# Kernel tuning notes

Measured on AMD Instinct MI355X. Metric: run time of the kernel, lower is better.

The kernel has to match this reference:

```python
import jax, jax.numpy as jnp
import numpy as np

NV = [12544, 6272, 3136, 1568, 784]  # vertex counts, fine -> coarse
SPIRAL = 9


def _grid_sample(im, grid):
    """Faithful port of the hand-rolled bilinear_grid_sample, align_corners=True.
    im: (n, c, h, w); grid: (n, gh, gw, 2) in [-1, 1]. Returns (n, c, gh*gw)."""
    n, c, h, w = im.shape
    gx = grid[..., 0].reshape(n, -1)
    gy = grid[..., 1].reshape(n, -1)
    x = (gx + 1) / 2 * (w - 1)
    y = (gy + 1) / 2 * (h - 1)
    x0 = jnp.floor(x); y0 = jnp.floor(y)
    x1 = x0 + 1; y1 = y0 + 1
    wa = (x1 - x) * (y1 - y)
    wb = (x1 - x) * (y - y0)
    wc = (x - x0) * (y1 - y)
    wd = (x - x0) * (y - y0)
    imp = jnp.pad(im, ((0, 0), (0, 0), (1, 1), (1, 1)))  # explicit zero pad as in source
    ph, pw = h + 2, w + 2
    x0i = jnp.clip(x0.astype(jnp.int32) + 1, 0, pw - 1)
    x1i = jnp.clip(x1.astype(jnp.int32) + 1, 0, pw - 1)
    y0i = jnp.clip(y0.astype(jnp.int32) + 1, 0, ph - 1)
    y1i = jnp.clip(y1.astype(jnp.int32) + 1, 0, ph - 1)
    impf = imp.reshape(n, c, -1)

    def gat(xi, yi):
        idx = xi + yi * pw  # (n, P)
        return jnp.take_along_axis(impf, idx[:, None, :], axis=2)  # (n, c, P)

    Ia = gat(x0i, y0i); Ib = gat(x0i, y1i); Ic = gat(x1i, y0i); Id = gat(x1i, y1i)
    return Ia * wa[:, None] + Ib * wb[:, None] + Ic * wc[:, None] + Id * wd[:, None]


def _pool(x, col, val):
    """Mesh up-pooling: gather columns, weight, and 3-way sum per output vertex.
    With row = repeat(arange(n_out), 3) the row_map built in __init__ is exactly
    arange(3*n_out).reshape(n_out, 3), so the three gathers reduce to reshape+sum."""
    out = x[:, col, :] * val[None, :, None]  # (B, 3*n_out, C)
    n_out = val.shape[0] // 3
    return out.reshape(x.shape[0], n_out, 3, x.shape[2]).sum(axis=2)


def _dsconv(x, idx, dw, pw):
    """Depthwise-separable spiral conv: gather spiral neighborhood, depthwise
    conv over spiral dim (per-channel), then 1x1 pointwise projection."""
    gsp = x[:, idx, :]                        # (B, N, S, Cin)
    y = jnp.einsum('bnsc,cs->bnc', gsp, dw)   # depthwise over spiral
    return y @ pw                             # (B, N, Cout)


def setup_inputs() -> dict:
    key = jax.random.key(0)
    ks = jax.random.split(key, 32)
    d = {}
    d['uv'] = jax.random.uniform(ks[0], (16, 64, 2), jnp.float32)
    d['feat'] = jax.random.normal(ks[1], (16, 256, 4, 4), jnp.float32)
    d['upsample'] = jax.random.normal(ks[2], (NV[4], 64), jnp.float32) * 0.01
    chs = [(256, 256), (256, 256), (256, 128), (128, 64)]
    for i, (ci, co) in enumerate(chs):
        d['dw%d' % i] = jax.random.normal(ks[3 + 2 * i], (ci, SPIRAL), jnp.float32) * (1.0 / SPIRAL)
        d['pw%d' % i] = jax.random.normal(ks[4 + 2 * i], (ci, co), jnp.float32) * (ci ** -0.5)
    d['dw_head'] = jax.random.normal(ks[11], (64, SPIRAL), jnp.float32) * (1.0 / SPIRAL)
    d['pw_head'] = jax.random.normal(ks[12], (64, 3), jnp.float32) * (64 ** -0.5)
    for j in range(4):
        n_out, n_in = NV[j], NV[j + 1]
        d['sp_idx_%d' % j] = jax.random.randint(ks[13 + j], (NV[j], SPIRAL), 0, NV[j], dtype=jnp.int32)
        d['up_col_%d' % j] = jax.random.randint(ks[17 + j], (3 * n_out,), 0, n_in, dtype=jnp.int32)
        d['up_val_%d' % j] = jax.random.uniform(ks[21 + j], (3 * n_out,), jnp.float32)
    return d


def reference(uv, feat, upsample, dw0, pw0, dw1, pw1, dw2, pw2, dw3, pw3, dw_head, pw_head,
              up_val_0, up_val_1, up_val_2, up_val_3,
              sp_idx_0, sp_idx_1, sp_idx_2, sp_idx_3,
              up_col_0, up_col_1, up_col_2, up_col_3):
    g = jnp.clip((uv - 0.5) * 2.0, -1.0, 1.0)[:, :, None, :]  # (B, P, 1, 2)
    x = _grid_sample(feat, g)            # (B, 256, P)
    x = x.transpose(0, 2, 1)             # (B, P, 256)
    x = jnp.einsum('vp,bpc->bvc', upsample, x)  # (B, 784, 256) coarse mesh feats
    specs = [(up_col_3, up_val_3, sp_idx_3, dw0, pw0),
             (up_col_2, up_val_2, sp_idx_2, dw1, pw1),
             (up_col_1, up_val_1, sp_idx_1, dw2, pw2),
             (up_col_0, up_val_0, sp_idx_0, dw3, pw3)]
    for col, val, idx, dw, pw in specs:
        x = _pool(x, col, val)
        x = jax.nn.relu(_dsconv(x, idx, dw, pw))
    return _dsconv(x, sp_idx_0, dw_head, pw_head)  # (B, 12544, 3)
```

## Files before the change

kernel.cpp:

```cpp
#include <hip/hip_runtime.h>


typedef _Float16 half8 __attribute__((ext_vector_type(8)));
typedef float    f32x4 __attribute__((ext_vector_type(4)));

__device__ __forceinline__ float4 ld4(const float* p) { return *(const float4*)p; }

__device__ __forceinline__ float lo16f(unsigned u) {
  _Float16 h; unsigned short s = (unsigned short)(u & 0xffffu);
  __builtin_memcpy(&h, &s, 2); return (float)h;
}
__device__ __forceinline__ float hi16f(unsigned u) {
  _Float16 h; unsigned short s = (unsigned short)(u >> 16);
  __builtin_memcpy(&h, &s, 2); return (float)h;
}
__device__ __forceinline__ float h2f(unsigned short s) {
  _Float16 h; __builtin_memcpy(&h, &s, 2); return (float)h;
}
__device__ __forceinline__ unsigned short hbits(float v) {
  _Float16 h = (_Float16)v; unsigned short u; __builtin_memcpy(&u, &h, 2); return u;
}
__device__ __forceinline__ unsigned pk2h(float a, float b) {
  return (unsigned)hbits(a) | ((unsigned)hbits(b) << 16);
}
__device__ __forceinline__ void split2h(float v, unsigned short& h, unsigned short& l) {
  _Float16 hf = (_Float16)v;
  float hif = (float)hf;
  _Float16 lf = (_Float16)((v - hif) * 2048.0f);
  __builtin_memcpy(&h, &hf, 2); __builtin_memcpy(&l, &lf, 2);
}
__device__ __forceinline__ void gload_lds16(const unsigned short* g, unsigned short* l) {
  __builtin_amdgcn_global_load_lds(
      (const __attribute__((address_space(1))) unsigned int*)g,
      (__attribute__((address_space(3))) unsigned int*)l, 16, 0, 0);
}

__global__ __launch_bounds__(256) void k_prep(
    const float* __restrict__ pw0, const float* __restrict__ pw1,
    const float* __restrict__ pw2, const float* __restrict__ pw3,
    unsigned short* __restrict__ dst)
{
  const int b = blockIdx.x, t = threadIdx.x;
  const float* src; int ci_sh, co, f, off;
  if (b < 256)      { src = pw0; ci_sh = 8; co = 256; f = b*256 + t;       off = 0; }
  else if (b < 512) { src = pw1; ci_sh = 8; co = 256; f = (b-256)*256 + t; off = 65536; }
  else if (b < 640) { src = pw2; ci_sh = 8; co = 128; f = (b-512)*256 + t; off = 131072; }
  else              { src = pw3; ci_sh = 7; co = 64;  f = (b-640)*256 + t; off = 163840; }
  const int n = f >> ci_sh, k = f & ((1 << ci_sh) - 1);
  float v = src[(size_t)k*co + n];
  unsigned short h, l; split2h(v, h, l);
  dst[off + f]          = h;
  dst[172032 + off + f] = l;
}

__global__ __launch_bounds__(256) void k_prep_head(
    const float* __restrict__ dwh, const float* __restrict__ pwh,
    unsigned short* __restrict__ dst)
{
  const int i = blockIdx.x*256 + threadIdx.x;
  const int n = i >> 6, c = i & 63;
  float v = 0.f;
  if (n < 27) v = dwh[c*9 + n/3] * pwh[c*3 + n%3];
  unsigned short h, l; split2h(v, h, l);
  dst[i] = h; dst[2048 + i] = l;
}

__global__ __launch_bounds__(256) void k_prep_dw(
    const float* __restrict__ dw0, const float* __restrict__ dw1,
    const float* __restrict__ dw2, const float* __restrict__ dw3,
    float* __restrict__ dst)
{
  const int i = blockIdx.x*256 + threadIdx.x;
  if (i >= 8064) return;
  const float* src; int rel, C, off;
  if (i < 2304)      { src = dw0; rel = i;        C = 256; off = 0; }
  else if (i < 4608) { src = dw1; rel = i - 2304; C = 256; off = 2304; }
  else if (i < 6912) { src = dw2; rel = i - 4608; C = 256; off = 4608; }
  else               { src = dw3; rel = i - 6912; C = 128; off = 6912; }
  const int s = rel / C, c = rel % C;
  dst[off + rel] = src[c*9 + s];
}

__global__ __launch_bounds__(256) void k_samp(
    const float* __restrict__ uv, const float* __restrict__ feat,
    unsigned short* __restrict__ xs)
{
  __shared__ float feat_l[256][17];
  const int tid = threadIdx.x;
  const int b   = blockIdx.x;

  const float* fr = feat + ((size_t)b*256 + tid)*16;
  #pragma unroll
  for (int i = 0; i < 16; i += 4) {
    float4 f = ld4(fr + i);
    feat_l[tid][i+0] = f.x; feat_l[tid][i+1] = f.y;
    feat_l[tid][i+2] = f.z; feat_l[tid][i+3] = f.w;
  }
  #pragma unroll 4
  for (int p = 0; p < 64; ++p) {
    float gx = uv[((size_t)b*64 + p)*2 + 0];
    float gy = uv[((size_t)b*64 + p)*2 + 1];
    gx = fminf(fmaxf((gx - 0.5f)*2.f, -1.f), 1.f);
    gy = fminf(fmaxf((gy - 0.5f)*2.f, -1.f), 1.f);
    float x = (gx + 1.f)*0.5f*3.f;
    float y = (gy + 1.f)*0.5f*3.f;
    float fx = floorf(x), fy = floorf(y);
    int ix0 = (int)fx, iy0 = (int)fy;
    float wx = x - fx, wy = y - fy;
    int ix1 = ix0 + 1 > 3 ? 3 : ix0 + 1;
    int iy1 = iy0 + 1 > 3 ? 3 : iy0 + 1;
    float v00 = feat_l[tid][iy0*4+ix0];
    float v01 = feat_l[tid][iy0*4+ix1];
    float v10 = feat_l[tid][iy1*4+ix0];
    float v11 = feat_l[tid][iy1*4+ix1];
    float xv = (1.f-wy)*((1.f-wx)*v00 + wx*v01) + wy*((1.f-wx)*v10 + wx*v11);
    xs[((size_t)b*64 + p)*256 + tid] = hbits(xv);
  }
}

__global__ __launch_bounds__(256) void k_up(
    const unsigned short* __restrict__ xs, const float* __restrict__ up,
    unsigned short* __restrict__ x0)
{
  const int tid = threadIdx.x;
  const int b   = blockIdx.y;
  const int v0  = blockIdx.x * 16;

  float acc[16];
  #pragma unroll
  for (int i = 0; i < 16; ++i) acc[i] = 0.f;

  #pragma unroll 8
  for (int p = 0; p < 64; ++p) {
    const float xv = h2f(xs[((size_t)b*64 + p)*256 + tid]);
    #pragma unroll
    for (int i = 0; i < 16; ++i)
      acc[i] += up[(size_t)(v0+i)*64 + p] * xv;
  }
  #pragma unroll
  for (int i = 0; i < 16; ++i)
    x0[((size_t)b*784 + v0 + i)*256 + tid] = hbits(acc[i]);
}

template<int C>
__global__ __launch_bounds__(256) void k_pool(
    const unsigned short* __restrict__ x, const int* __restrict__ col,
    const float* __restrict__ val, unsigned short* __restrict__ out,
    int Vin, int Vout)
{
  constexpr int KGc = C/8;
  constexpr int UPB = 2*KGc;
  const int bp = blockIdx.x & 7;
  const int v0 = (blockIdx.x >> 3) * 8;
  const int t  = threadIdx.x;

  #pragma unroll
  for (int i = 0; i < (8*UPB)/256; ++i) {
    const int id = t + i*256;
    const int vl = id / UPB;
    const int rem = id - vl*UPB;
    const int bl = rem / KGc;
    const int kg = rem - bl*KGc;
    const int v  = v0 + vl;
    const int b  = 2*bp + bl;
    const int c0 = col[3*v+0], c1 = col[3*v+1], c2 = col[3*v+2];
    const float w0 = val[3*v+0], w1 = val[3*v+1], w2 = val[3*v+2];
    const uint4 A = *(const uint4*)(x + ((size_t)b*Vin + c0)*C + 8*kg);
    const uint4 B = *(const uint4*)(x + ((size_t)b*Vin + c1)*C + 8*kg);
    const uint4 Cv= *(const uint4*)(x + ((size_t)b*Vin + c2)*C + 8*kg);
    uint4 R;
    R.x = pk2h(w0*lo16f(A.x)+w1*lo16f(B.x)+w2*lo16f(Cv.x),
               w0*hi16f(A.x)+w1*hi16f(B.x)+w2*hi16f(Cv.x));
    R.y = pk2h(w0*lo16f(A.y)+w1*lo16f(B.y)+w2*lo16f(Cv.y),
               w0*hi16f(A.y)+w1*hi16f(B.y)+w2*hi16f(Cv.y));
    R.z = pk2h(w0*lo16f(A.z)+w1*lo16f(B.z)+w2*lo16f(Cv.z),
               w0*hi16f(A.z)+w1*hi16f(B.z)+w2*hi16f(Cv.z));
    R.w = pk2h(w0*lo16f(A.w)+w1*lo16f(B.w)+w2*lo16f(Cv.w),
               w0*hi16f(A.w)+w1*hi16f(B.w)+w2*hi16f(Cv.w));
    *(uint4*)(out + ((size_t)b*Vout + v)*C + 8*kg) = R;
  }
}

template<int CI>
__global__ __launch_bounds__(256) void k_dw(
    const unsigned short* __restrict__ pin, const int* __restrict__ idx,
    const float* __restrict__ dwT, unsigned short* __restrict__ aout, int V)
{
  constexpr int KG  = CI/8;
  constexpr int VPB = (CI==256) ? 8 : 16;
  constexpr int HV  = VPB/2;

  const int t    = threadIdx.x;
  const int bp   = blockIdx.x & 7;
  const int vg   = blockIdx.x >> 3;
  const int kg   = t & (KG - 1);
  const int rest = t / KG;
  const int bl   = rest & 1;
  const int vbase= rest >> 1;
  const int va   = vg*VPB + vbase;
  const int vb2  = va + HV;
  const int b    = 2*bp + bl;

  const unsigned short* base = pin + (size_t)b*V*CI + 8*kg;
  float y0[8], y1[8];
  #pragma unroll
  for (int j = 0; j < 8; ++j) { y0[j] = 0.f; y1[j] = 0.f; }

  #pragma unroll
  for (int s = 0; s < 9; ++s) {
    const float4 wa = *(const float4*)(dwT + s*CI + 8*kg);
    const float4 wb = *(const float4*)(dwT + s*CI + 8*kg + 4);
    const uint4 g0 = *(const uint4*)(base + (size_t)idx[va *9 + s]*CI);
    const uint4 g1 = *(const uint4*)(base + (size_t)idx[vb2*9 + s]*CI);
    y0[0] += wa.x*lo16f(g0.x); y0[1] += wa.y*hi16f(g0.x);
    y0[2] += wa.z*lo16f(g0.y); y0[3] += wa.w*hi16f(g0.y);
    y0[4] += wb.x*lo16f(g0.z); y0[5] += wb.y*hi16f(g0.z);
    y0[6] += wb.z*lo16f(g0.w); y0[7] += wb.w*hi16f(g0.w);
    y1[0] += wa.x*lo16f(g1.x); y1[1] += wa.y*hi16f(g1.x);
    y1[2] += wa.z*lo16f(g1.y); y1[3] += wa.w*hi16f(g1.y);
    y1[4] += wb.x*lo16f(g1.z); y1[5] += wb.y*hi16f(g1.z);
    y1[6] += wb.z*lo16f(g1.w); y1[7] += wb.w*hi16f(g1.w);
  }
  uint4 p0, p1;
  p0.x = pk2h(y0[0], y0[1]); p0.y = pk2h(y0[2], y0[3]);
  p0.z = pk2h(y0[4], y0[5]); p0.w = pk2h(y0[6], y0[7]);
  p1.x = pk2h(y1[0], y1[1]); p1.y = pk2h(y1[2], y1[3]);
  p1.z = pk2h(y1[4], y1[5]); p1.w = pk2h(y1[6], y1[7]);
  *(uint4*)(aout + (size_t)(va *16 + b)*CI + 8*kg) = p0;
  *(uint4*)(aout + (size_t)(vb2*16 + b)*CI + 8*kg) = p1;
}

template<int CI, int COT, int NTW, bool RELU>
__global__ __launch_bounds__(256) void k_gemm(
    const unsigned short* __restrict__ A,
    const unsigned short* __restrict__ bhp, const unsigned short* __restrict__ blp,
    unsigned short* __restrict__ out, int Vout)
{
  constexpr int CHUNKS = CI/32;
  constexpr int NCOL   = NTW*64;
  constexpr int OROW   = NCOL + 8;
  constexpr int ABYTES = 64*CI*2;
  constexpr int OBYTES = 64*OROW*2;
  constexpr int LBYTES = (ABYTES > OBYTES) ? ABYTES : OBYTES;
  constexpr int SLOTS  = ABYTES/16;

  __shared__ __align__(16) char lds_raw[LBYTES];
  unsigned short* a_l = (unsigned short*)lds_raw;

  const int t  = threadIdx.x;
  const size_t m0 = (size_t)blockIdx.x * 64;
  const int co0 = blockIdx.y * NCOL;
  const int w = t >> 6, l = t & 15, q = (t >> 4) & 3;
  const int lane6 = t & 63;

  #pragma unroll
  for (int r = 0; r < SLOTS/256; ++r) {
    const int s    = t + r*256;
    const int c    = s >> 8;
    const int mt   = (s >> 6) & 3;
    const int ql   = s & 63;
    const int m    = mt*16 + (ql & 15);
    const int koff = c*32 + (ql >> 4)*8;
    gload_lds16(A + (m0 + m)*CI + koff, a_l + (size_t)s*8);
  }
  __syncthreads();

  f32x4 ah[4][NTW], ax[4][NTW];
  #pragma unroll
  for (int mt = 0; mt < 4; ++mt)
    #pragma unroll
    for (int n = 0; n < NTW; ++n)
      #pragma unroll
      for (int r = 0; r < 4; ++r) { ah[mt][n][r] = 0.f; ax[mt][n][r] = 0.f; }

  #pragma unroll
  for (int c = 0; c < CHUNKS; ++c) {
    const int k0 = c*32 + q*8;
    half8 fa[4], fbh[NTW], fbl[NTW];
    #pragma unroll
    for (int mt = 0; mt < 4; ++mt)
      fa[mt] = *(const half8*)(a_l + (size_t)(c*256 + mt*64 + lane6)*8);
    #pragma unroll
    for (int n = 0; n < NTW; ++n) {
      const size_t boff = (size_t)(co0 + (w*NTW + n)*16 + l)*CI + k0;
      fbh[n] = *(const half8*)(bhp + boff);
      fbl[n] = *(const half8*)(blp + boff);
    }
    #pragma unroll
    for (int mt = 0; mt < 4; ++mt)
      #pragma unroll
      for (int n = 0; n < NTW; ++n) {
        ah[mt][n] = __builtin_amdgcn_mfma_f32_16x16x32_f16(fa[mt], fbh[n], ah[mt][n], 0, 0, 0);
        ax[mt][n] = __builtin_amdgcn_mfma_f32_16x16x32_f16(fa[mt], fbl[n], ax[mt][n], 0, 0, 0);
      }
  }

  __syncthreads();
  unsigned short (*ot)[OROW] = (unsigned short (*)[OROW])lds_raw;
  #pragma unroll
  for (int mt = 0; mt < 4; ++mt)
    #pragma unroll
    for (int n = 0; n < NTW; ++n) {
      const int colg = (w*NTW + n)*16 + l;
      #pragma unroll
      for (int r = 0; r < 4; ++r) {
        const int row = mt*16 + q*4 + r;
        float v = ah[mt][n][r] + ax[mt][n][r] * (1.0f/2048.0f);
        if (RELU) v = fmaxf(v, 0.f);
        ot[row][colg] = hbits(v);
      }
    }
  __syncthreads();
  constexpr int PR = NCOL/8;
  #pragma unroll
  for (int i = 0; i < (64*PR)/256; ++i) {
    const int item = t + i*256;
    const int r  = item / PR;
    const int cp = (item % PR)*8;
    const size_t m = m0 + r;
    const int v = (int)(m >> 4), b = (int)(m & 15);
    *(uint4*)(out + ((size_t)b*Vout + v)*COT + co0 + cp) = *(const uint4*)&ot[r][cp];
  }
}

__global__ __launch_bounds__(256) void k_headz(
    const unsigned short* __restrict__ A,
    const unsigned short* __restrict__ bhT, const unsigned short* __restrict__ blT,
    float* __restrict__ z)
{
  __shared__ float zt[4][32][16];

  const int t = threadIdx.x;
  const size_t m0 = (size_t)blockIdx.x * 64;
  const int w = t >> 6, l = t & 15, q = (t >> 4) & 3;

  f32x4 acch[2], accl[2];
  #pragma unroll
  for (int n = 0; n < 2; ++n)
    #pragma unroll
    for (int r = 0; r < 4; ++r) { acch[n][r] = 0.f; accl[n][r] = 0.f; }

  const size_t m = m0 + w*16 + l;
  const size_t arow = ((m & 15)*12544 + (m >> 4))*64;
  #pragma unroll
  for (int c = 0; c < 2; ++c) {
    const int k0 = c*32 + q*8;
    half8 fa = *(const half8*)(A + arow + k0);
    #pragma unroll
    for (int n = 0; n < 2; ++n) {
      half8 fbh = *(const half8*)(bhT + (size_t)(n*16 + l)*64 + k0);
      half8 fbl = *(const half8*)(blT + (size_t)(n*16 + l)*64 + k0);
      acch[n] = __builtin_amdgcn_mfma_f32_16x16x32_f16(fa, fbh, acch[n], 0, 0, 0);
      accl[n] = __builtin_amdgcn_mfma_f32_16x16x32_f16(fa, fbl, accl[n], 0, 0, 0);
    }
  }

  #pragma unroll
  for (int n = 0; n < 2; ++n)
    #pragma unroll
    for (int r = 0; r < 4; ++r)
      zt[w][n*16 + l][q*4 + r] = acch[n][r] + accl[n][r] * (1.0f/2048.0f);
  __syncthreads();

  const size_t u0 = m0 >> 4;
  #pragma unroll
  for (int i = 0; i < 7; ++i) {
    const int item = t + i*256;
    if (item < 1728) {
      const int ul  = item / 432;
      const int rem = item - ul*432;
      const int s   = rem / 48;
      const int bj  = rem - s*48;
      const int b   = bj / 3;
      const int j   = bj - b*3;
      z[(u0 + ul)*432 + rem] = zt[ul][s*3 + j][b];
    }
  }
}

__global__ __launch_bounds__(256) void k_head2(
    const float* __restrict__ z, const int* __restrict__ idx,
    float* __restrict__ out, int nvert)
{
  const int w    = threadIdx.x >> 6;
  const int lane = threadIdx.x & 63;
  const int v    = blockIdx.x*4 + w;
  if (lane < 48) {
    float acc = 0.f;
    #pragma unroll
    for (int s = 0; s < 9; ++s) {
      const int u = idx[v*9 + s];
      acc += z[(size_t)u*432 + s*48 + lane];
    }
    const int b = lane / 3, j = lane - b*3;
    out[((size_t)b*nvert + v)*3 + j] = acc;
  }
}

extern "C" void kernel_launch(void* const* d_in, const int* in_sizes, int n_in,
                              void* d_out, int out_size, void* d_ws, size_t ws_size,
                              hipStream_t stream)
{
  const float* uv   = (const float*)d_in[0];
  const float* feat = (const float*)d_in[1];
  const float* up   = (const float*)d_in[2];
  const float* dw0  = (const float*)d_in[3];
  const float* pw0  = (const float*)d_in[4];
  const float* dw1  = (const float*)d_in[5];
  const float* pw1  = (const float*)d_in[6];
  const float* dw2  = (const float*)d_in[7];
  const float* pw2  = (const float*)d_in[8];
  const float* dw3  = (const float*)d_in[9];
  const float* pw3  = (const float*)d_in[10];
  const float* dwh  = (const float*)d_in[11];
  const float* pwh  = (const float*)d_in[12];
  const int*   sp0  = (const int*)d_in[13];
  const int*   col0 = (const int*)d_in[14];
  const float* val0 = (const float*)d_in[15];
  const int*   sp1  = (const int*)d_in[16];
  const int*   col1 = (const int*)d_in[17];
  const float* val1 = (const float*)d_in[18];
  const int*   sp2  = (const int*)d_in[19];
  const int*   col2 = (const int*)d_in[20];
  const float* val2 = (const float*)d_in[21];
  const int*   sp3  = (const int*)d_in[22];
  const int*   col3 = (const int*)d_in[23];
  const float* val3 = (const float*)d_in[24];

  unsigned short* bufA  = (unsigned short*)d_ws;
  unsigned short* bufB  = (unsigned short*)((char*)d_ws + 25690112);
  unsigned short* bufC  = (unsigned short*)((char*)d_ws + 77070336);
  unsigned short* pwT   = (unsigned short*)((char*)d_ws + 128450560);
  unsigned short* bhead = (unsigned short*)((char*)d_ws + 129138688);
  float*          dwT   = (float*)((char*)d_ws + 129155072);
  float*          zbuf  = (float*)((char*)d_ws + 129187328);
  unsigned short* xs    = (unsigned short*)((char*)d_ws + 150863360);
  float* outp = (float*)d_out;

  unsigned short* h0 = pwT;            unsigned short* L0 = pwT + 172032;
  unsigned short* h1 = pwT + 65536;    unsigned short* L1 = L0 + 65536;
  unsigned short* h2 = pwT + 131072;   unsigned short* L2 = L0 + 131072;
  unsigned short* h3 = pwT + 163840;   unsigned short* L3 = L0 + 163840;
  unsigned short* hh = bhead;          unsigned short* Lh = bhead + 2048;
  float* dwT0 = dwT;          float* dwT1 = dwT + 2304;
  float* dwT2 = dwT + 4608;   float* dwT3 = dwT + 6912;

  k_prep<<<672, 256, 0, stream>>>(pw0, pw1, pw2, pw3, pwT);
  k_prep_head<<<8, 256, 0, stream>>>(dwh, pwh, bhead);
  k_prep_dw<<<32, 256, 0, stream>>>(dw0, dw1, dw2, dw3, dwT);
  k_samp<<<16, 256, 0, stream>>>(uv, feat, xs);
  k_up<<<dim3(49,16,1), 256, 0, stream>>>(xs, up, bufA);

  k_pool<256><<<1568, 256, 0, stream>>>(bufA, col3, val3, bufB, 784, 1568);
  k_dw<256><<<1568, 256, 0, stream>>>(bufB, sp3, dwT0, bufC, 1568);
  k_gemm<256,256,2,true><<<dim3(392,2), 256, 0, stream>>>(bufC, h0, L0, bufA, 1568);

  k_pool<256><<<3136, 256, 0, stream>>>(bufA, col2, val2, bufB, 1568, 3136);
  k_dw<256><<<3136, 256, 0, stream>>>(bufB, sp2, dwT1, bufC, 3136);
  k_gemm<256,256,2,true><<<dim3(784,2), 256, 0, stream>>>(bufC, h1, L1, bufA, 3136);

  k_pool<256><<<6272, 256, 0, stream>>>(bufA, col1, val1, bufB, 3136, 6272);
  k_dw<256><<<6272, 256, 0, stream>>>(bufB, sp1, dwT2, bufC, 6272);
  k_gemm<256,128,2,true><<<dim3(1568,1), 256, 0, stream>>>(bufC, h2, L2, bufA, 6272);

  k_pool<128><<<12544, 256, 0, stream>>>(bufA, col0, val0, bufB, 6272, 12544);
  k_dw<128><<<6272, 256, 0, stream>>>(bufB, sp0, dwT3, bufC, 12544);
  k_gemm<128,64,1,true><<<dim3(3136,1), 256, 0, stream>>>(bufC, h3, L3, bufA, 12544);

  k_headz<<<3136, 256, 0, stream>>>(bufA, hh, Lh, zbuf);
  k_head2<<<3136, 256, 0, stream>>>(zbuf, sp0, outp, 12544);
}
```

Baseline: 433.7 us.

## Fuse depthwise spiral conv and pointwise GEMM for the two finest levels

```diff
diff --git a/kernel.cpp b/kernel.cpp
--- a/kernel.cpp
+++ b/kernel.cpp
@@ -320,6 +320,115 @@
     const size_t m = m0 + r;
     const int v = (int)(m >> 4), b = (int)(m & 15);
     *(uint4*)(out + ((size_t)b*Vout + v)*COT + co0 + cp) = *(const uint4*)&ot[r][cp];
+  }
+}
+
+template<int CI, int CO, int NTW, bool RELU>
+__global__ __launch_bounds__(256) void k_fuse(
+    const unsigned short* __restrict__ pin, const int* __restrict__ idx,
+    const float* __restrict__ dwT,
+    const unsigned short* __restrict__ bhp, const unsigned short* __restrict__ blp,
+    unsigned short* __restrict__ out, int Vin, int Vout, int VG)
+{
+  constexpr int KG     = CI/8;
+  constexpr int VPT    = KG/4;
+  constexpr int AROW   = CI + 8;
+  constexpr int OROW   = CO + 8;
+  constexpr int CHUNKS = CI/32;
+
+  __shared__ __align__(16) unsigned short a_l[64][AROW];
+
+  const int t = threadIdx.x;
+  const int x = blockIdx.x & 7;
+  const int i = blockIdx.x >> 3;
+  const int phase = (i >= VG) ? 1 : 0;
+  const int vg = i - phase*VG;
+  const int b  = x + 8*phase;
+  const int v0 = vg*64;
+
+  {
+    const int kg  = t & (KG - 1);
+    const int vt0 = (t/KG) * VPT;
+    const unsigned short* base = pin + (size_t)b*Vin*CI + 8*kg;
+    #pragma unroll
+    for (int vv = 0; vv < VPT; ++vv) {
+      const int vloc = vt0 + vv;
+      const int* ip = idx + (size_t)(v0 + vloc)*9;
+      float y[8];
+      #pragma unroll
+      for (int j = 0; j < 8; ++j) y[j] = 0.f;
+      #pragma unroll
+      for (int s = 0; s < 9; ++s) {
+        const float4 wa = *(const float4*)(dwT + s*CI + 8*kg);
+        const float4 wb = *(const float4*)(dwT + s*CI + 8*kg + 4);
+        const uint4 g = *(const uint4*)(base + (size_t)ip[s]*CI);
+        y[0] += wa.x*lo16f(g.x); y[1] += wa.y*hi16f(g.x);
+        y[2] += wa.z*lo16f(g.y); y[3] += wa.w*hi16f(g.y);
+        y[4] += wb.x*lo16f(g.z); y[5] += wb.y*hi16f(g.z);
+        y[6] += wb.z*lo16f(g.w); y[7] += wb.w*hi16f(g.w);
+      }
+      uint4 pk;
+      pk.x = pk2h(y[0], y[1]); pk.y = pk2h(y[2], y[3]);
+      pk.z = pk2h(y[4], y[5]); pk.w = pk2h(y[6], y[7]);
+      *(uint4*)&a_l[vloc][8*kg] = pk;
+    }
+  }
+  __syncthreads();
+
+  const int w = t >> 6, l = t & 15, q = (t >> 4) & 3;
+  f32x4 ah[4][NTW], ax[4][NTW];
+  #pragma unroll
+  for (int mt = 0; mt < 4; ++mt)
+    #pragma unroll
+    for (int n = 0; n < NTW; ++n)
+      #pragma unroll
+      for (int r = 0; r < 4; ++r) { ah[mt][n][r] = 0.f; ax[mt][n][r] = 0.f; }
+
+  #pragma unroll
+  for (int c = 0; c < CHUNKS; ++c) {
+    const int k0 = c*32 + q*8;
+    half8 fa[4], fbh[NTW], fbl[NTW];
+    #pragma unroll
+    for (int mt = 0; mt < 4; ++mt)
+      fa[mt] = *(const half8*)&a_l[mt*16 + l][k0];
+    #pragma unroll
+    for (int n = 0; n < NTW; ++n) {
+      const size_t boff = (size_t)((w*NTW + n)*16 + l)*CI + k0;
+      fbh[n] = *(const half8*)(bhp + boff);
+      fbl[n] = *(const half8*)(blp + boff);
+    }
+    #pragma unroll
+    for (int mt = 0; mt < 4; ++mt)
+      #pragma unroll
+      for (int n = 0; n < NTW; ++n) {
+        ah[mt][n] = __builtin_amdgcn_mfma_f32_16x16x32_f16(fa[mt], fbh[n], ah[mt][n], 0, 0, 0);
+        ax[mt][n] = __builtin_amdgcn_mfma_f32_16x16x32_f16(fa[mt], fbl[n], ax[mt][n], 0, 0, 0);
+      }
+  }
+
+  __syncthreads();
+  unsigned short (*ot)[OROW] = (unsigned short (*)[OROW])&a_l[0][0];
+  #pragma unroll
+  for (int mt = 0; mt < 4; ++mt)
+    #pragma unroll
+    for (int n = 0; n < NTW; ++n) {
+      const int colg = (w*NTW + n)*16 + l;
+      #pragma unroll
+      for (int r = 0; r < 4; ++r) {
+        const int row = mt*16 + q*4 + r;
+        float v = ah[mt][n][r] + ax[mt][n][r] * (1.0f/2048.0f);
+        if (RELU) v = fmaxf(v, 0.f);
+        ot[row][colg] = hbits(v);
+      }
+    }
+  __syncthreads();
+  constexpr int PR = CO/8;
+  #pragma unroll
+  for (int ii = 0; ii < (64*PR)/256; ++ii) {
+    const int item = t + ii*256;
+    const int r  = item / PR;
+    const int cp = (item % PR)*8;
+    *(uint4*)(out + ((size_t)b*Vout + v0 + r)*CO + cp) = *(const uint4*)&ot[r][cp];
   }
 }
 
@@ -460,12 +569,10 @@
   k_gemm<256,256,2,true><<<dim3(784,2), 256, 0, stream>>>(bufC, h1, L1, bufA, 3136);
 
   k_pool<256><<<6272, 256, 0, stream>>>(bufA, col1, val1, bufB, 3136, 6272);
-  k_dw<256><<<6272, 256, 0, stream>>>(bufB, sp1, dwT2, bufC, 6272);
-  k_gemm<256,128,2,true><<<dim3(1568,1), 256, 0, stream>>>(bufC, h2, L2, bufA, 6272);
+  k_fuse<256,128,2,true><<<16*98, 256, 0, stream>>>(bufB, sp1, dwT2, h2, L2, bufA, 6272, 6272, 98);
 
   k_pool<128><<<12544, 256, 0, stream>>>(bufA, col0, val0, bufB, 6272, 12544);
-  k_dw<128><<<6272, 256, 0, stream>>>(bufB, sp0, dwT3, bufC, 12544);
-  k_gemm<128,64,1,true><<<dim3(3136,1), 256, 0, stream>>>(bufC, h3, L3, bufA, 12544);
+  k_fuse<128,64,1,true><<<16*196, 256, 0, stream>>>(bufB, sp0, dwT3, h3, L3, bufA, 12544, 12544, 196);
 
   k_headz<<<3136, 256, 0, stream>>>(bufA, hh, Lh, zbuf);
   k_head2<<<3136, 256, 0, stream>>>(zbuf, sp0, outp, 12544);
```

New measurement: 623.8 us. +43.8%, slower.
